# Optimization experiments

Measured on AMD Instinct MI355X. Metric: run time of the kernel, lower is better.

The kernel has to match this reference:

```python
import jax, jax.numpy as jnp
import numpy as np

IN_CH, HID, OUT = 128, 128, 47

def _sage_conv(x_src, x_dst, src, dst, n_dst, Wl, bl, Wr):
    # mean aggregation of source features onto destination nodes
    msg_sum = jax.ops.segment_sum(x_src[src], dst, num_segments=n_dst)
    deg = jax.ops.segment_sum(jnp.ones((src.shape[0],), x_src.dtype), dst, num_segments=n_dst)
    agg = msg_sum / jnp.maximum(deg, 1.0)[:, None]
    return agg @ Wl + bl + x_dst @ Wr


def setup_inputs() -> dict:
    key = jax.random.key(0)
    ks = jax.random.split(key, 12)
    N0, N1, N2 = 200000, 100000, 20000
    E0, E1 = 1600000, 320000
    def glorot(k, fan_in, fan_out):
        s = jnp.sqrt(6.0 / (fan_in + fan_out))
        return jax.random.uniform(k, (fan_in, fan_out), jnp.float32, -s, s)
    return {
        'x': jax.random.normal(ks[0], (N0, IN_CH), jnp.float32),
        'src0': jax.random.randint(ks[1], (E0,), 0, N0),
        'dst0': jax.random.randint(ks[2], (E0,), 0, N1),
        'src1': jax.random.randint(ks[3], (E1,), 0, N1),
        'dst1': jax.random.randint(ks[4], (E1,), 0, N2),
        'n1': N1,
        'n2': N2,
        'Wl0': glorot(ks[5], IN_CH, HID),
        'bl0': jnp.zeros((HID,), jnp.float32),
        'Wr0': glorot(ks[6], IN_CH, HID),
        'Wl1': glorot(ks[7], HID, OUT),
        'bl1': jnp.zeros((OUT,), jnp.float32),
        'Wr1': glorot(ks[8], HID, OUT),
    }


def reference(x, src0, dst0, src1, dst1, n1, n2, Wl0, bl0, Wr0, Wl1, bl1, Wr1):
    # layer 0: bipartite SAGEConv + relu (dropout is identity in eval mode)
    h = _sage_conv(x, x[:n1], src0, dst0, n1, Wl0, bl0, Wr0)
    h = jax.nn.relu(h)
    # layer 1: SAGEConv to output classes
    out = _sage_conv(h, h[:n2], src1, dst1, n2, Wl1, bl1, Wr1)
    return jax.nn.log_softmax(out, axis=-1)
```

## Files before the change

### kernel.cpp

```cpp
#include <hip/hip_runtime.h>
#include <hip/hip_bf16.h>
#include <math.h>

#define N1_ROWS 100000
#define N2_ROWS 20000
#define CH 128
#define OUTC 47
#define BSH 7
#define BROWS 128
#define CAP 2560
#define NBMX 1024
#define SCHUNK 4096

typedef __attribute__((ext_vector_type(8))) short short8;
typedef __attribute__((ext_vector_type(4))) float floatx4;

__device__ inline ushort f2b(float f) {
    union { __hip_bfloat16 b; ushort u; } cv;
    cv.b = __float2bfloat16(f);
    return cv.u;
}
__device__ inline float b2f_lo(uint u) { return __uint_as_float(u << 16); }
__device__ inline float b2f_hi(uint u) { return __uint_as_float(u & 0xffff0000u); }

__device__ inline void scatter_body(
    const int* __restrict__ src, const int* __restrict__ dst,
    uint* __restrict__ gcur, uint* __restrict__ ebuf, int E, int NB,
    int sb, uint* hist, uint* runb)
{
    const int base = sb * SCHUNK;
    const int t = threadIdx.x;

    uint d[16], s[16];
    bool ok[4];
    #pragma unroll
    for (int j = 0; j < 4; ++j) {
        int e = base + j * 1024 + t * 4;
        ok[j] = (e < E);
        if (ok[j]) {
            uint4 dv = *(const uint4*)(dst + e);
            uint4 sv = *(const uint4*)(src + e);
            d[j*4+0] = dv.x; d[j*4+1] = dv.y; d[j*4+2] = dv.z; d[j*4+3] = dv.w;
            s[j*4+0] = sv.x; s[j*4+1] = sv.y; s[j*4+2] = sv.z; s[j*4+3] = sv.w;
        }
    }

    for (int b = t; b < NBMX; b += 256) hist[b] = 0;
    __syncthreads();
    #pragma unroll
    for (int j = 0; j < 4; ++j)
        if (ok[j]) {
            #pragma unroll
            for (int k = 0; k < 4; ++k) atomicAdd(&hist[d[j*4+k] >> BSH], 1u);
        }
    __syncthreads();
    for (int b = t; b < NB; b += 256) {
        uint c = hist[b];
        runb[b] = c ? atomicAdd(&gcur[b], c) : 0u;
        hist[b] = 0;
    }
    __syncthreads();
    #pragma unroll
    for (int j = 0; j < 4; ++j)
        if (ok[j]) {
            #pragma unroll
            for (int k = 0; k < 4; ++k) {
                uint dd = d[j*4+k];
                uint b = dd >> BSH;
                uint off = runb[b] + atomicAdd(&hist[b], 1u);
                if (off < CAP)
                    ebuf[(size_t)b * CAP + off] = ((dd & (BROWS - 1u)) << 18) | s[j*4+k];
            }
        }
}

__global__ __launch_bounds__(256) void prep(
    const float* __restrict__ x, ushort* __restrict__ xb, int n4,
    const int* __restrict__ src0, const int* __restrict__ dst0,
    uint* __restrict__ gcur0, uint* __restrict__ ebuf0, int E0, int NB0,
    const int* __restrict__ src1, const int* __restrict__ dst1,
    uint* __restrict__ gcur1, uint* __restrict__ ebuf1, int E1, int NB1,
    const float* __restrict__ Wl0, const float* __restrict__ Wr0,
    const float* __restrict__ Wl1, const float* __restrict__ Wr1,
    const float* __restrict__ bl1,
    ushort* __restrict__ W0p, ushort* __restrict__ W1p, float* __restrict__ bl1p,
    int CB, int S0, int S1)
{
    __shared__ uint hist[NBMX];
    __shared__ uint runb[NBMX];
    int blk = blockIdx.x;
    if (blk < S0) {
        scatter_body(src0, dst0, gcur0, ebuf0, E0, NB0, blk, hist, runb);
    } else if (blk < S0 + S1) {
        scatter_body(src1, dst1, gcur1, ebuf1, E1, NB1, blk - S0, hist, runb);
    } else if (blk == S0 + S1) {
        int t = threadIdx.x;
        for (int c = t; c < 4096; c += 256) {
            int n = c & 127; int kb = (c >> 7) & 15; int p = c >> 11;
            const float* W = p ? Wr0 : Wl0;
            __align__(16) ushort tmp[8];
            #pragma unroll
            for (int i = 0; i < 8; ++i) tmp[i] = f2b(W[(kb * 8 + i) * CH + n]);
            *(uint4*)(W0p + (size_t)c * 8) = *(const uint4*)tmp;
        }
    } else if (blk == S0 + S1 + 1) {
        int t = threadIdx.x;
        for (int c = t; c < 1536; c += 256) {
            int n = c % 48; int kb = (c / 48) & 15; int p = c / 768;
            const float* W = p ? Wr1 : Wl1;
            __align__(16) ushort tmp[8];
            #pragma unroll
            for (int i = 0; i < 8; ++i)
                tmp[i] = (n < OUTC) ? f2b(W[(kb * 8 + i) * OUTC + n]) : (ushort)0;
            *(uint4*)(W1p + (size_t)c * 8) = *(const uint4*)tmp;
        }
        if (t < 48) bl1p[t] = (t < OUTC) ? bl1[t] : -3.0e38f;
    } else {
        int i = (blk - S0 - S1 - 2) * 256 + threadIdx.x;
        if (i < n4) {
            float4 v = ((const float4*)x)[i];
            ushort4 o;
            o.x = f2b(v.x); o.y = f2b(v.y); o.z = f2b(v.z); o.w = f2b(v.w);
            ((ushort4*)xb)[i] = o;
        }
    }
}

__global__ __launch_bounds__(512) void csr_gather(
    const uint* __restrict__ ebuf0, const uint* __restrict__ gcur0,
    const ushort* __restrict__ xb, ushort* __restrict__ aggb, int NB0, int n1,
    const uint* __restrict__ ebuf1, const uint* __restrict__ gcur1,
    int* __restrict__ idx1, int* __restrict__ deg1, int* __restrict__ rs1,
    int NB1, int n2)
{
    int t = threadIdx.x;
    __shared__ uint idxl[CAP];
    __shared__ uint hist[BROWS];
    __shared__ uint sc[BROWS];
    __shared__ uint lrs[BROWS];
    __shared__ uint degl[BROWS];
    __shared__ uint psc[256];

    int b = blockIdx.x;
    if (b < NB0) {
        uint cnt = gcur0[b]; if (cnt > CAP) cnt = CAP;
        size_t bin = (size_t)b * CAP;

        if (t < BROWS) hist[t] = 0;
        __syncthreads();
        for (uint i0 = 0; i0 < cnt; i0 += 2048) {
            uint i = i0 + t * 4;
            uint v0 = 0, v1 = 0, v2 = 0, v3 = 0; int nv = 0;
            if (i + 3 < cnt) {
                uint4 vv = *(const uint4*)(ebuf0 + bin + i);
                v0 = vv.x; v1 = vv.y; v2 = vv.z; v3 = vv.w; nv = 4;
            } else if (i < cnt) {
                nv = (int)(cnt - i);
                v0 = ebuf0[bin + i];
                if (nv > 1) v1 = ebuf0[bin + i + 1];
                if (nv > 2) v2 = ebuf0[bin + i + 2];
            }
            if (nv > 0) atomicAdd(&hist[v0 >> 18], 1u);
            if (nv > 1) atomicAdd(&hist[v1 >> 18], 1u);
            if (nv > 2) atomicAdd(&hist[v2 >> 18], 1u);
            if (nv > 3) atomicAdd(&hist[v3 >> 18], 1u);
        }
        __syncthreads();
        uint hv = 0;
        if (t < BROWS) { hv = hist[t]; sc[t] = hv; }
        __syncthreads();
        for (int off = 1; off < BROWS; off <<= 1) {
            uint val = 0;
            if (t < BROWS && t >= off) val = sc[t - off];
            __syncthreads();
            if (t < BROWS) sc[t] += val;
            __syncthreads();
        }
        if (t < BROWS) { lrs[t] = sc[t] - hv; degl[t] = hv; hist[t] = 0; }
        __syncthreads();
        for (uint i0 = 0; i0 < cnt; i0 += 2048) {
            uint i = i0 + t * 4;
            uint v0 = 0, v1 = 0, v2 = 0, v3 = 0; int nv = 0;
            if (i + 3 < cnt) {
                uint4 vv = *(const uint4*)(ebuf0 + bin + i);
                v0 = vv.x; v1 = vv.y; v2 = vv.z; v3 = vv.w; nv = 4;
            } else if (i < cnt) {
                nv = (int)(cnt - i);
                v0 = ebuf0[bin + i];
                if (nv > 1) v1 = ebuf0[bin + i + 1];
                if (nv > 2) v2 = ebuf0[bin + i + 2];
            }
            if (nv > 0) { uint r = v0 >> 18; idxl[lrs[r] + atomicAdd(&hist[r], 1u)] = v0 & 0x3FFFFu; }
            if (nv > 1) { uint r = v1 >> 18; idxl[lrs[r] + atomicAdd(&hist[r], 1u)] = v1 & 0x3FFFFu; }
            if (nv > 2) { uint r = v2 >> 18; idxl[lrs[r] + atomicAdd(&hist[r], 1u)] = v2 & 0x3FFFFu; }
            if (nv > 3) { uint r = v3 >> 18; idxl[lrs[r] + atomicAdd(&hist[r], 1u)] = v3 & 0x3FFFFu; }
        }
        __syncthreads();

        int wave = t >> 6, lane = t & 63;
        const int g  = lane >> 4;
        const int sl = lane & 15;
        const int gid = wave * 4 + g;
        const uint4* x4 = (const uint4*)xb;
        #pragma unroll 1
        for (int k = 0; k < 4; ++k) {
            int r = gid + 32 * k;
            int row = (b << BSH) + r;
            if (row >= n1) break;
            int start = (int)lrs[r];
            int cnt_r = (int)degl[r];
            float a0 = 0.f, a1 = 0.f, a2 = 0.f, a3 = 0.f;
            float a4 = 0.f, a5 = 0.f, a6 = 0.f, a7 = 0.f;
            int i = 0;
            for (; i + 3 < cnt_r; i += 4) {
                uint s0 = idxl[start + i];
                uint s1 = idxl[start + i + 1];
                uint s2 = idxl[start + i + 2];
                uint s3 = idxl[start + i + 3];
                uint4 v0 = x4[(size_t)s0 * 16 + sl];
                uint4 v1 = x4[(size_t)s1 * 16 + sl];
                uint4 v2 = x4[(size_t)s2 * 16 + sl];
                uint4 v3 = x4[(size_t)s3 * 16 + sl];
                a0 += (b2f_lo(v0.x) + b2f_lo(v1.x)) + (b2f_lo(v2.x) + b2f_lo(v3.x));
                a1 += (b2f_hi(v0.x) + b2f_hi(v1.x)) + (b2f_hi(v2.x) + b2f_hi(v3.x));
                a2 += (b2f_lo(v0.y) + b2f_lo(v1.y)) + (b2f_lo(v2.y) + b2f_lo(v3.y));
                a3 += (b2f_hi(v0.y) + b2f_hi(v1.y)) + (b2f_hi(v2.y) + b2f_hi(v3.y));
                a4 += (b2f_lo(v0.z) + b2f_lo(v1.z)) + (b2f_lo(v2.z) + b2f_lo(v3.z));
                a5 += (b2f_hi(v0.z) + b2f_hi(v1.z)) + (b2f_hi(v2.z) + b2f_hi(v3.z));
                a6 += (b2f_lo(v0.w) + b2f_lo(v1.w)) + (b2f_lo(v2.w) + b2f_lo(v3.w));
                a7 += (b2f_hi(v0.w) + b2f_hi(v1.w)) + (b2f_hi(v2.w) + b2f_hi(v3.w));
            }
            for (; i < cnt_r; ++i) {
                uint s0 = idxl[start + i];
                uint4 v0 = x4[(size_t)s0 * 16 + sl];
                a0 += b2f_lo(v0.x); a1 += b2f_hi(v0.x);
                a2 += b2f_lo(v0.y); a3 += b2f_hi(v0.y);
                a4 += b2f_lo(v0.z); a5 += b2f_hi(v0.z);
                a6 += b2f_lo(v0.w); a7 += b2f_hi(v0.w);
            }
            float inv = 1.0f / fmaxf((float)cnt_r, 1.0f);
            uint4 o;
            o.x = (uint)f2b(a0 * inv) | ((uint)f2b(a1 * inv) << 16);
            o.y = (uint)f2b(a2 * inv) | ((uint)f2b(a3 * inv) << 16);
            o.z = (uint)f2b(a4 * inv) | ((uint)f2b(a5 * inv) << 16);
            o.w = (uint)f2b(a6 * inv) | ((uint)f2b(a7 * inv) << 16);
            ((uint4*)aggb)[(size_t)row * 16 + sl] = o;
        }
    } else {
        b -= NB0;
        if (t < 256) {
            uint c = (t < NB1) ? gcur1[t] : 0u; if (c > CAP) c = CAP;
            psc[t] = c;
        }
        __syncthreads();
        for (int off = 1; off < 256; off <<= 1) {
            uint val = 0;
            if (t < 256 && t >= off) val = psc[t - off];
            __syncthreads();
            if (t < 256) psc[t] += val;
            __syncthreads();
        }
        uint cnt = gcur1[b]; if (cnt > CAP) cnt = CAP;
        uint bout = psc[b] - cnt;
        size_t bin = (size_t)b * CAP;
        int row0 = b << BSH;
        int nrows = n2 - row0; if (nrows > BROWS) nrows = BROWS;

        if (t < BROWS) hist[t] = 0;
        __syncthreads();
        for (uint i0 = 0; i0 < cnt; i0 += 2048) {
            uint i = i0 + t * 4;
            uint v0 = 0, v1 = 0, v2 = 0, v3 = 0; int nv = 0;
            if (i + 3 < cnt) {
                uint4 vv = *(const uint4*)(ebuf1 + bin + i);
                v0 = vv.x; v1 = vv.y; v2 = vv.z; v3 = vv.w; nv = 4;
            } else if (i < cnt) {
                nv = (int)(cnt - i);
                v0 = ebuf1[bin + i];
                if (nv > 1) v1 = ebuf1[bin + i + 1];
                if (nv > 2) v2 = ebuf1[bin + i + 2];
            }
            if (nv > 0) atomicAdd(&hist[v0 >> 18], 1u);
            if (nv > 1) atomicAdd(&hist[v1 >> 18], 1u);
            if (nv > 2) atomicAdd(&hist[v2 >> 18], 1u);
            if (nv > 3) atomicAdd(&hist[v3 >> 18], 1u);
        }
        __syncthreads();
        uint hv = 0;
        if (t < BROWS) { hv = hist[t]; sc[t] = hv; }
        __syncthreads();
        for (int off = 1; off < BROWS; off <<= 1) {
            uint val = 0;
            if (t < BROWS && t >= off) val = sc[t - off];
            __syncthreads();
            if (t < BROWS) sc[t] += val;
            __syncthreads();
        }
        if (t < BROWS) {
            uint lb = sc[t] - hv;
            lrs[t] = lb;
            if (t < nrows) { deg1[row0 + t] = (int)hv; rs1[row0 + t] = (int)(bout + lb); }
            hist[t] = 0;
        }
        __syncthreads();
        for (uint i0 = 0; i0 < cnt; i0 += 2048) {
            uint i = i0 + t * 4;
            uint v0 = 0, v1 = 0, v2 = 0, v3 = 0; int nv = 0;
            if (i + 3 < cnt) {
                uint4 vv = *(const uint4*)(ebuf1 + bin + i);
                v0 = vv.x; v1 = vv.y; v2 = vv.z; v3 = vv.w; nv = 4;
            } else if (i < cnt) {
                nv = (int)(cnt - i);
                v0 = ebuf1[bin + i];
                if (nv > 1) v1 = ebuf1[bin + i + 1];
                if (nv > 2) v2 = ebuf1[bin + i + 2];
            }
            if (nv > 0) { uint r = v0 >> 18; idxl[lrs[r] + atomicAdd(&hist[r], 1u)] = v0 & 0x3FFFFu; }
            if (nv > 1) { uint r = v1 >> 18; idxl[lrs[r] + atomicAdd(&hist[r], 1u)] = v1 & 0x3FFFFu; }
            if (nv > 2) { uint r = v2 >> 18; idxl[lrs[r] + atomicAdd(&hist[r], 1u)] = v2 & 0x3FFFFu; }
            if (nv > 3) { uint r = v3 >> 18; idxl[lrs[r] + atomicAdd(&hist[r], 1u)] = v3 & 0x3FFFFu; }
        }
        __syncthreads();
        for (uint i = t; i < cnt; i += 512) idx1[bout + i] = (int)idxl[i];
    }
}

__global__ __launch_bounds__(256) void gather_mean_bb(
    const ushort* __restrict__ xb,
    const int* __restrict__ idx,
    const int* __restrict__ rs,
    const int* __restrict__ deg,
    ushort* __restrict__ aggb,
    int n)
{
    int lane = threadIdx.x & 63;
    int wave = threadIdx.x >> 6;
    const int g  = lane >> 4;
    const int sl = lane & 15;
    int row = blockIdx.x * 16 + wave * 4 + g;
    if (row >= n) return;
    int start = rs[row];
    int cnt = deg[row];
    const uint4* x4 = (const uint4*)xb;
    float a0 = 0.f, a1 = 0.f, a2 = 0.f, a3 = 0.f;
    float a4 = 0.f, a5 = 0.f, a6 = 0.f, a7 = 0.f;
    int i = 0;
    for (; i + 3 < cnt; i += 4) {
        int s0 = idx[start + i];
        int s1 = idx[start + i + 1];
        int s2 = idx[start + i + 2];
        int s3 = idx[start + i + 3];
        uint4 v0 = x4[(size_t)s0 * 16 + sl];
        uint4 v1 = x4[(size_t)s1 * 16 + sl];
        uint4 v2 = x4[(size_t)s2 * 16 + sl];
        uint4 v3 = x4[(size_t)s3 * 16 + sl];
        a0 += (b2f_lo(v0.x) + b2f_lo(v1.x)) + (b2f_lo(v2.x) + b2f_lo(v3.x));
        a1 += (b2f_hi(v0.x) + b2f_hi(v1.x)) + (b2f_hi(v2.x) + b2f_hi(v3.x));
        a2 += (b2f_lo(v0.y) + b2f_lo(v1.y)) + (b2f_lo(v2.y) + b2f_lo(v3.y));
        a3 += (b2f_hi(v0.y) + b2f_hi(v1.y)) + (b2f_hi(v2.y) + b2f_hi(v3.y));
        a4 += (b2f_lo(v0.z) + b2f_lo(v1.z)) + (b2f_lo(v2.z) + b2f_lo(v3.z));
        a5 += (b2f_hi(v0.z) + b2f_hi(v1.z)) + (b2f_hi(v2.z) + b2f_hi(v3.z));
        a6 += (b2f_lo(v0.w) + b2f_lo(v1.w)) + (b2f_lo(v2.w) + b2f_lo(v3.w));
        a7 += (b2f_hi(v0.w) + b2f_hi(v1.w)) + (b2f_hi(v2.w) + b2f_hi(v3.w));
    }
    for (; i < cnt; ++i) {
        int s0 = idx[start + i];
        uint4 v0 = x4[(size_t)s0 * 16 + sl];
        a0 += b2f_lo(v0.x); a1 += b2f_hi(v0.x);
        a2 += b2f_lo(v0.y); a3 += b2f_hi(v0.y);
        a4 += b2f_lo(v0.z); a5 += b2f_hi(v0.z);
        a6 += b2f_lo(v0.w); a7 += b2f_hi(v0.w);
    }
    float inv = 1.0f / fmaxf((float)cnt, 1.0f);
    uint4 o;
    o.x = (uint)f2b(a0 * inv) | ((uint)f2b(a1 * inv) << 16);
    o.y = (uint)f2b(a2 * inv) | ((uint)f2b(a3 * inv) << 16);
    o.z = (uint)f2b(a4 * inv) | ((uint)f2b(a5 * inv) << 16);
    o.w = (uint)f2b(a6 * inv) | ((uint)f2b(a7 * inv) << 16);
    ((uint4*)aggb)[(size_t)row * 16 + sl] = o;
}

#define TM 128
__global__ __launch_bounds__(256) void gemm_mfma(
    const ushort* __restrict__ Apan,
    const ushort* __restrict__ Bpan,
    const ushort* __restrict__ Wp,
    const float* __restrict__ bias,
    ushort* __restrict__ H,
    int rows)
{
    __shared__ __align__(16) ushort As[16384];
    __shared__ __align__(16) ushort Ws[16384];

    const int tid = threadIdx.x;
    const int lane = tid & 63;
    const int wave = tid >> 6;
    const int q = lane >> 4;
    const int ln = lane & 15;
    const int rbase = blockIdx.x * TM;
    const int mrow = wave * 32;

    floatx4 acc[2][8];
    #pragma unroll
    for (int i = 0; i < 2; ++i)
        #pragma unroll
        for (int j = 0; j < 8; ++j)
            acc[i][j] = (floatx4)0.0f;

    #pragma unroll 1
    for (int phase = 0; phase < 2; ++phase) {
        const ushort* Ag = phase ? Bpan : Apan;

        {
            int m0 = tid & 15;
            int c  = tid >> 4;
            #pragma unroll
            for (int j = 0; j < 8; ++j) {
                int m = m0 + 16 * j;
                uint4 v = *(const uint4*)(Ag + (size_t)(rbase + m) * CH + c * 8);
                *(uint4*)(As + ((size_t)c * 128 + m) * 8) = v;
            }
        }
        {
            const uint4* Wg4 = (const uint4*)(Wp + phase * 16384);
            uint4* Ws4 = (uint4*)Ws;
            for (int i = tid; i < 2048; i += 256) Ws4[i] = Wg4[i];
        }
        __syncthreads();

        #pragma unroll
        for (int k = 0; k < 4; ++k) {
            int kb = k * 4 + q;
            short8 b[8];
            #pragma unroll
            for (int nt = 0; nt < 8; ++nt)
                b[nt] = *(const short8*)(Ws + ((size_t)kb * 128 + nt * 16 + ln) * 8);
            #pragma unroll
            for (int mt = 0; mt < 2; ++mt) {
                short8 a = *(const short8*)(As + ((size_t)kb * 128 + mrow + mt * 16 + ln) * 8);
                #pragma unroll
                for (int nt = 0; nt < 8; ++nt)
                    acc[mt][nt] = __builtin_amdgcn_mfma_f32_16x16x32_bf16(
                        a, b[nt], acc[mt][nt], 0, 0, 0);
            }
        }
        __syncthreads();
    }

    float bj[8];
    #pragma unroll
    for (int nt = 0; nt < 8; ++nt) bj[nt] = bias[nt * 16 + ln];

    #pragma unroll
    for (int mt = 0; mt < 2; ++mt) {
        #pragma unroll
        for (int r = 0; r < 4; ++r) {
            int grow = rbase + mrow + mt * 16 + q * 4 + r;
            if (grow < rows) {
                #pragma unroll
                for (int nt = 0; nt < 8; ++nt) {
                    float v = acc[mt][nt][r] + bj[nt];
                    v = fmaxf(v, 0.0f);
                    H[(size_t)grow * CH + nt * 16 + ln] = f2b(v);
                }
            }
        }
    }
}

__global__ __launch_bounds__(256) void gemm_mfma_l1(
    const ushort* __restrict__ Apan,
    const ushort* __restrict__ Bpan,
    const ushort* __restrict__ Wp,
    const float* __restrict__ biasp,
    float* __restrict__ out,
    int rows)
{
    __shared__ __align__(16) ushort As[16384];
    __shared__ __align__(16) ushort Ws[6144];

    const int tid = threadIdx.x;
    const int lane = tid & 63;
    const int wave = tid >> 6;
    const int q = lane >> 4;
    const int ln = lane & 15;
    const int rbase = blockIdx.x * TM;
    const int mrow = wave * 32;

    floatx4 acc[2][3];
    #pragma unroll
    for (int i = 0; i < 2; ++i)
        #pragma unroll
        for (int j = 0; j < 3; ++j)
            acc[i][j] = (floatx4)0.0f;

    #pragma unroll 1
    for (int phase = 0; phase < 2; ++phase) {
        const ushort* Ag = phase ? Bpan : Apan;
        {
            int m0 = tid & 15;
            int c  = tid >> 4;
            #pragma unroll
            for (int j = 0; j < 8; ++j) {
                int m = m0 + 16 * j;
                uint4 v = *(const uint4*)(Ag + (size_t)(rbase + m) * CH + c * 8);
                *(uint4*)(As + ((size_t)c * 128 + m) * 8) = v;
            }
        }
        {
            const uint4* Wg4 = (const uint4*)(Wp + phase * 6144);
            uint4* Ws4 = (uint4*)Ws;
            for (int i = tid; i < 768; i += 256) Ws4[i] = Wg4[i];
        }
        __syncthreads();

        #pragma unroll
        for (int k = 0; k < 4; ++k) {
            int kb = k * 4 + q;
            short8 b0 = *(const short8*)(Ws + ((size_t)kb * 48 +  0 + ln) * 8);
            short8 b1 = *(const short8*)(Ws + ((size_t)kb * 48 + 16 + ln) * 8);
            short8 b2 = *(const short8*)(Ws + ((size_t)kb * 48 + 32 + ln) * 8);
            #pragma unroll
            for (int mt = 0; mt < 2; ++mt) {
                short8 a = *(const short8*)(As + ((size_t)kb * 128 + mrow + mt * 16 + ln) * 8);
                acc[mt][0] = __builtin_amdgcn_mfma_f32_16x16x32_bf16(a, b0, acc[mt][0], 0, 0, 0);
                acc[mt][1] = __builtin_amdgcn_mfma_f32_16x16x32_bf16(a, b1, acc[mt][1], 0, 0, 0);
                acc[mt][2] = __builtin_amdgcn_mfma_f32_16x16x32_bf16(a, b2, acc[mt][2], 0, 0, 0);
            }
        }
        __syncthreads();
    }

    float b0 = biasp[ln], b1 = biasp[16 + ln], b2 = biasp[32 + ln];

    #pragma unroll
    for (int mt = 0; mt < 2; ++mt) {
        #pragma unroll
        for (int r = 0; r < 4; ++r) {
            int grow = rbase + mrow + mt * 16 + q * 4 + r;
            float v0 = acc[mt][0][r] + b0;
            float v1 = acc[mt][1][r] + b1;
            float v2 = acc[mt][2][r] + b2;
            float mx = fmaxf(v0, fmaxf(v1, v2));
            #pragma unroll
            for (int off = 1; off < 16; off <<= 1) mx = fmaxf(mx, __shfl_xor(mx, off));
            float s = expf(v0 - mx) + expf(v1 - mx) + expf(v2 - mx);
            #pragma unroll
            for (int off = 1; off < 16; off <<= 1) s += __shfl_xor(s, off);
            float ls = mx + logf(s);
            if (grow < rows) {
                out[(size_t)grow * OUTC + ln] = v0 - ls;
                out[(size_t)grow * OUTC + 16 + ln] = v1 - ls;
                if (32 + ln < OUTC) out[(size_t)grow * OUTC + 32 + ln] = v2 - ls;
            }
        }
    }
}

extern "C" void kernel_launch(void* const* d_in, const int* in_sizes, int n_in,
                              void* d_out, int out_size, void* d_ws, size_t ws_size,
                              hipStream_t stream) {
    const float* x    = (const float*)d_in[0];
    const int*   src0 = (const int*)d_in[1];
    const int*   dst0 = (const int*)d_in[2];
    const int*   src1 = (const int*)d_in[3];
    const int*   dst1 = (const int*)d_in[4];
    const float* Wl0  = (const float*)d_in[7];
    const float* bl0  = (const float*)d_in[8];
    const float* Wr0  = (const float*)d_in[9];
    const float* Wl1  = (const float*)d_in[10];
    const float* bl1  = (const float*)d_in[11];
    const float* Wr1  = (const float*)d_in[12];
    float* out = (float*)d_out;

    const int E0 = in_sizes[1];
    const int E1 = in_sizes[3];
    const int n0 = in_sizes[0] / CH;
    const int n1 = N1_ROWS, n2 = N2_ROWS;
    const int n1pad = ((n1 + TM - 1) / TM) * TM;
    const int n2pad = ((n2 + TM - 1) / TM) * TM;
    const int NB0 = (n1 + BROWS - 1) >> BSH;
    const int NB1 = (n2 + BROWS - 1) >> BSH;

    ushort* xb   = (ushort*)d_ws;
    ushort* aggb = xb + (size_t)n0 * CH;
    ushort* h    = aggb + (size_t)n1pad * CH;
    ushort* W0p  = h + (size_t)n1 * CH;
    ushort* W1p  = W0p + 32768;
    float*  bl1p = (float*)(W1p + 12288);
    int*    idx1 = (int*)(bl1p + 48);
    int*    deg1 = idx1 + E1;
    int*    rs1  = deg1 + n2;
    uint*   gcur0 = (uint*)(rs1 + n2);
    uint*   gcur1 = gcur0 + NBMX;

    uint* ebuf0 = (uint*)h;
    uint* ebuf1 = (uint*)h + (size_t)NB0 * CAP;
    ushort* agg1b = aggb;

    const int n4 = n0 * CH / 4;
    const int CB = (n4 + 255) / 256;
    const int S0 = (E0 + SCHUNK - 1) / SCHUNK;
    const int S1 = (E1 + SCHUNK - 1) / SCHUNK;

    hipMemsetAsync(gcur0, 0, 2 * NBMX * sizeof(uint), stream);
    prep<<<S0 + S1 + 2 + CB, 256, 0, stream>>>(
        x, xb, n4,
        src0, dst0, gcur0, ebuf0, E0, NB0,
        src1, dst1, gcur1, ebuf1, E1, NB1,
        Wl0, Wr0, Wl1, Wr1, bl1, W0p, W1p, bl1p,
        CB, S0, S1);
    csr_gather<<<NB0 + NB1, 512, 0, stream>>>(
        ebuf0, gcur0, xb, aggb, NB0, n1,
        ebuf1, gcur1, idx1, deg1, rs1, NB1, n2);
    gemm_mfma<<<n1pad / TM, 256, 0, stream>>>(aggb, xb, W0p, bl0, h, n1);
    gather_mean_bb<<<(n2 + 15) / 16, 256, 0, stream>>>(h, idx1, rs1, deg1, agg1b, n2);
    gemm_mfma_l1<<<n2pad / TM, 256, 0, stream>>>(agg1b, h, W1p, bl1p, out, n2);
}
```

Before: 316.2 us.

## Fuse per-block CSR gather with MFMA GEMM for both SAGE layers

Each 128-row destination block now builds its local CSR, gathers and averages neighbor features straight into shared memory in the MFMA A-layout, then runs the two-phase GEMM (aggregate @ Wl plus self @ Wr) in the same kernel. This removes the global round trip of the aggregated features and the layer-1 idx/deg/rowstart buffers, and cuts four kernel launches to two. The edge buffers move to their own workspace region because h is now written while they are still needed. In exchange each block uses much more shared memory (about 64KB extra), which lowers occupancy during the latency-bound gather, and the GEMM now uses 8 waves with 16 rows each.

```diff
diff --git a/kernel.cpp b/kernel.cpp
--- a/kernel.cpp
+++ b/kernel.cpp
@@ -126,12 +126,12 @@
     }
 }
 
-__global__ __launch_bounds__(512) void csr_gather(
-    const uint* __restrict__ ebuf0, const uint* __restrict__ gcur0,
-    const ushort* __restrict__ xb, ushort* __restrict__ aggb, int NB0, int n1,
-    const uint* __restrict__ ebuf1, const uint* __restrict__ gcur1,
-    int* __restrict__ idx1, int* __restrict__ deg1, int* __restrict__ rs1,
-    int NB1, int n2)
+__global__ __launch_bounds__(512) void fused0(
+    const uint* __restrict__ ebuf, const uint* __restrict__ gcur,
+    const ushort* __restrict__ xb,
+    const ushort* __restrict__ Wp,
+    const float* __restrict__ bias,
+    ushort* __restrict__ H, int n1)
 {
     int t = threadIdx.x;
     __shared__ uint idxl[CAP];
@@ -139,74 +139,80 @@
     __shared__ uint sc[BROWS];
     __shared__ uint lrs[BROWS];
     __shared__ uint degl[BROWS];
-    __shared__ uint psc[256];
+    __shared__ __align__(16) ushort As[16384];
+    __shared__ __align__(16) ushort Ws[16384];
 
     int b = blockIdx.x;
-    if (b < NB0) {
-        uint cnt = gcur0[b]; if (cnt > CAP) cnt = CAP;
-        size_t bin = (size_t)b * CAP;
-
-        if (t < BROWS) hist[t] = 0;
+    uint cnt = gcur[b]; if (cnt > CAP) cnt = CAP;
+    size_t bin = (size_t)b * CAP;
+
+    {
+        const uint4* Wg4 = (const uint4*)Wp;
+        uint4* Ws4 = (uint4*)Ws;
+        for (int i = t; i < 2048; i += 512) Ws4[i] = Wg4[i];
+    }
+
+    if (t < BROWS) hist[t] = 0;
+    __syncthreads();
+    for (uint i0 = 0; i0 < cnt; i0 += 2048) {
+        uint i = i0 + t * 4;
+        uint v0 = 0, v1 = 0, v2 = 0, v3 = 0; int nv = 0;
+        if (i + 3 < cnt) {
+            uint4 vv = *(const uint4*)(ebuf + bin + i);
+            v0 = vv.x; v1 = vv.y; v2 = vv.z; v3 = vv.w; nv = 4;
+        } else if (i < cnt) {
+            nv = (int)(cnt - i);
+            v0 = ebuf[bin + i];
+            if (nv > 1) v1 = ebuf[bin + i + 1];
+            if (nv > 2) v2 = ebuf[bin + i + 2];
+        }
+        if (nv > 0) atomicAdd(&hist[v0 >> 18], 1u);
+        if (nv > 1) atomicAdd(&hist[v1 >> 18], 1u);
+        if (nv > 2) atomicAdd(&hist[v2 >> 18], 1u);
+        if (nv > 3) atomicAdd(&hist[v3 >> 18], 1u);
+    }
+    __syncthreads();
+    uint hv = 0;
+    if (t < BROWS) { hv = hist[t]; sc[t] = hv; }
+    __syncthreads();
+    for (int off = 1; off < BROWS; off <<= 1) {
+        uint val = 0;
+        if (t < BROWS && t >= off) val = sc[t - off];
         __syncthreads();
-        for (uint i0 = 0; i0 < cnt; i0 += 2048) {
-            uint i = i0 + t * 4;
-            uint v0 = 0, v1 = 0, v2 = 0, v3 = 0; int nv = 0;
-            if (i + 3 < cnt) {
-                uint4 vv = *(const uint4*)(ebuf0 + bin + i);
-                v0 = vv.x; v1 = vv.y; v2 = vv.z; v3 = vv.w; nv = 4;
-            } else if (i < cnt) {
-                nv = (int)(cnt - i);
-                v0 = ebuf0[bin + i];
-                if (nv > 1) v1 = ebuf0[bin + i + 1];
-                if (nv > 2) v2 = ebuf0[bin + i + 2];
-            }
-            if (nv > 0) atomicAdd(&hist[v0 >> 18], 1u);
-            if (nv > 1) atomicAdd(&hist[v1 >> 18], 1u);
-            if (nv > 2) atomicAdd(&hist[v2 >> 18], 1u);
-            if (nv > 3) atomicAdd(&hist[v3 >> 18], 1u);
-        }
+        if (t < BROWS) sc[t] += val;
         __syncthreads();
-        uint hv = 0;
-        if (t < BROWS) { hv = hist[t]; sc[t] = hv; }
-        __syncthreads();
-        for (int off = 1; off < BROWS; off <<= 1) {
-            uint val = 0;
-            if (t < BROWS && t >= off) val = sc[t - off];
-            __syncthreads();
-            if (t < BROWS) sc[t] += val;
-            __syncthreads();
-        }
-        if (t < BROWS) { lrs[t] = sc[t] - hv; degl[t] = hv; hist[t] = 0; }
-        __syncthreads();
-        for (uint i0 = 0; i0 < cnt; i0 += 2048) {
-            uint i = i0 + t * 4;
-            uint v0 = 0, v1 = 0, v2 = 0, v3 = 0; int nv = 0;
-            if (i + 3 < cnt) {
-                uint4 vv = *(const uint4*)(ebuf0 + bin + i);
-                v0 = vv.x; v1 = vv.y; v2 = vv.z; v3 = vv.w; nv = 4;
-            } else if (i < cnt) {
-                nv = (int)(cnt - i);
-                v0 = ebuf0[bin + i];
-                if (nv > 1) v1 = ebuf0[bin + i + 1];
-                if (nv > 2) v2 = ebuf0[bin + i + 2];
-            }
-            if (nv > 0) { uint r = v0 >> 18; idxl[lrs[r] + atomicAdd(&hist[r], 1u)] = v0 & 0x3FFFFu; }
-            if (nv > 1) { uint r = v1 >> 18; idxl[lrs[r] + atomicAdd(&hist[r], 1u)] = v1 & 0x3FFFFu; }
-            if (nv > 2) { uint r = v2 >> 18; idxl[lrs[r] + atomicAdd(&hist[r], 1u)] = v2 & 0x3FFFFu; }
-            if (nv > 3) { uint r = v3 >> 18; idxl[lrs[r] + atomicAdd(&hist[r], 1u)] = v3 & 0x3FFFFu; }
-        }
-        __syncthreads();
-
-        int wave = t >> 6, lane = t & 63;
-        const int g  = lane >> 4;
-        const int sl = lane & 15;
-        const int gid = wave * 4 + g;
-        const uint4* x4 = (const uint4*)xb;
-        #pragma unroll 1
-        for (int k = 0; k < 4; ++k) {
-            int r = gid + 32 * k;
-            int row = (b << BSH) + r;
-            if (row >= n1) break;
+    }
+    if (t < BROWS) { lrs[t] = sc[t] - hv; degl[t] = hv; hist[t] = 0; }
+    __syncthreads();
+    for (uint i0 = 0; i0 < cnt; i0 += 2048) {
+        uint i = i0 + t * 4;
+        uint v0 = 0, v1 = 0, v2 = 0, v3 = 0; int nv = 0;
+        if (i + 3 < cnt) {
+            uint4 vv = *(const uint4*)(ebuf + bin + i);
+            v0 = vv.x; v1 = vv.y; v2 = vv.z; v3 = vv.w; nv = 4;
+        } else if (i < cnt) {
+            nv = (int)(cnt - i);
+            v0 = ebuf[bin + i];
+            if (nv > 1) v1 = ebuf[bin + i + 1];
+            if (nv > 2) v2 = ebuf[bin + i + 2];
+        }
+        if (nv > 0) { uint r = v0 >> 18; idxl[lrs[r] + atomicAdd(&hist[r], 1u)] = v0 & 0x3FFFFu; }
+        if (nv > 1) { uint r = v1 >> 18; idxl[lrs[r] + atomicAdd(&hist[r], 1u)] = v1 & 0x3FFFFu; }
+        if (nv > 2) { uint r = v2 >> 18; idxl[lrs[r] + atomicAdd(&hist[r], 1u)] = v2 & 0x3FFFFu; }
+        if (nv > 3) { uint r = v3 >> 18; idxl[lrs[r] + atomicAdd(&hist[r], 1u)] = v3 & 0x3FFFFu; }
+    }
+    __syncthreads();
+
+    int wave = t >> 6, lane = t & 63;
+    const int g  = lane >> 4;
+    const int sl = lane & 15;
+    const int gid = wave * 4 + g;
+    const uint4* x4 = (const uint4*)xb;
+    #pragma unroll 1
+    for (int k = 0; k < 4; ++k) {
+        int r = gid + 32 * k;
+        int row = (b << BSH) + r;
+        if (row < n1) {
             int start = (int)lrs[r];
             int cnt_r = (int)degl[r];
             float a0 = 0.f, a1 = 0.f, a2 = 0.f, a3 = 0.f;
@@ -244,315 +250,254 @@
             o.y = (uint)f2b(a2 * inv) | ((uint)f2b(a3 * inv) << 16);
             o.z = (uint)f2b(a4 * inv) | ((uint)f2b(a5 * inv) << 16);
             o.w = (uint)f2b(a6 * inv) | ((uint)f2b(a7 * inv) << 16);
-            ((uint4*)aggb)[(size_t)row * 16 + sl] = o;
-        }
-    } else {
-        b -= NB0;
-        if (t < 256) {
-            uint c = (t < NB1) ? gcur1[t] : 0u; if (c > CAP) c = CAP;
-            psc[t] = c;
-        }
-        __syncthreads();
-        for (int off = 1; off < 256; off <<= 1) {
-            uint val = 0;
-            if (t < 256 && t >= off) val = psc[t - off];
-            __syncthreads();
-            if (t < 256) psc[t] += val;
-            __syncthreads();
-        }
-        uint cnt = gcur1[b]; if (cnt > CAP) cnt = CAP;
-        uint bout = psc[b] - cnt;
-        size_t bin = (size_t)b * CAP;
-        int row0 = b << BSH;
-        int nrows = n2 - row0; if (nrows > BROWS) nrows = BROWS;
-
-        if (t < BROWS) hist[t] = 0;
-        __syncthreads();
-        for (uint i0 = 0; i0 < cnt; i0 += 2048) {
-            uint i = i0 + t * 4;
-            uint v0 = 0, v1 = 0, v2 = 0, v3 = 0; int nv = 0;
-            if (i + 3 < cnt) {
-                uint4 vv = *(const uint4*)(ebuf1 + bin + i);
-                v0 = vv.x; v1 = vv.y; v2 = vv.z; v3 = vv.w; nv = 4;
-            } else if (i < cnt) {
-                nv = (int)(cnt - i);
-                v0 = ebuf1[bin + i];
-                if (nv > 1) v1 = ebuf1[bin + i + 1];
-                if (nv > 2) v2 = ebuf1[bin + i + 2];
-            }
-            if (nv > 0) atomicAdd(&hist[v0 >> 18], 1u);
-            if (nv > 1) atomicAdd(&hist[v1 >> 18], 1u);
-            if (nv > 2) atomicAdd(&hist[v2 >> 18], 1u);
-            if (nv > 3) atomicAdd(&hist[v3 >> 18], 1u);
-        }
-        __syncthreads();
-        uint hv = 0;
-        if (t < BROWS) { hv = hist[t]; sc[t] = hv; }
-        __syncthreads();
-        for (int off = 1; off < BROWS; off <<= 1) {
-            uint val = 0;
-            if (t < BROWS && t >= off) val = sc[t - off];
-            __syncthreads();
-            if (t < BROWS) sc[t] += val;
-            __syncthreads();
-        }
-        if (t < BROWS) {
-            uint lb = sc[t] - hv;
-            lrs[t] = lb;
-            if (t < nrows) { deg1[row0 + t] = (int)hv; rs1[row0 + t] = (int)(bout + lb); }
-            hist[t] = 0;
-        }
-        __syncthreads();
-        for (uint i0 = 0; i0 < cnt; i0 += 2048) {
-            uint i = i0 + t * 4;
-            uint v0 = 0, v1 = 0, v2 = 0, v3 = 0; int nv = 0;
-            if (i + 3 < cnt) {
-                uint4 vv = *(const uint4*)(ebuf1 + bin + i);
-                v0 = vv.x; v1 = vv.y; v2 = vv.z; v3 = vv.w; nv = 4;
-            } else if (i < cnt) {
-                nv = (int)(cnt - i);
-                v0 = ebuf1[bin + i];
-                if (nv > 1) v1 = ebuf1[bin + i + 1];
-                if (nv > 2) v2 = ebuf1[bin + i + 2];
-            }
-            if (nv > 0) { uint r = v0 >> 18; idxl[lrs[r] + atomicAdd(&hist[r], 1u)] = v0 & 0x3FFFFu; }
-            if (nv > 1) { uint r = v1 >> 18; idxl[lrs[r] + atomicAdd(&hist[r], 1u)] = v1 & 0x3FFFFu; }
-            if (nv > 2) { uint r = v2 >> 18; idxl[lrs[r] + atomicAdd(&hist[r], 1u)] = v2 & 0x3FFFFu; }
-            if (nv > 3) { uint r = v3 >> 18; idxl[lrs[r] + atomicAdd(&hist[r], 1u)] = v3 & 0x3FFFFu; }
-        }
-        __syncthreads();
-        for (uint i = t; i < cnt; i += 512) idx1[bout + i] = (int)idxl[i];
-    }
-}
-
-__global__ __launch_bounds__(256) void gather_mean_bb(
-    const ushort* __restrict__ xb,
-    const int* __restrict__ idx,
-    const int* __restrict__ rs,
-    const int* __restrict__ deg,
-    ushort* __restrict__ aggb,
-    int n)
-{
-    int lane = threadIdx.x & 63;
-    int wave = threadIdx.x >> 6;
-    const int g  = lane >> 4;
-    const int sl = lane & 15;
-    int row = blockIdx.x * 16 + wave * 4 + g;
-    if (row >= n) return;
-    int start = rs[row];
-    int cnt = deg[row];
-    const uint4* x4 = (const uint4*)xb;
-    float a0 = 0.f, a1 = 0.f, a2 = 0.f, a3 = 0.f;
-    float a4 = 0.f, a5 = 0.f, a6 = 0.f, a7 = 0.f;
-    int i = 0;
-    for (; i + 3 < cnt; i += 4) {
-        int s0 = idx[start + i];
-        int s1 = idx[start + i + 1];
-        int s2 = idx[start + i + 2];
-        int s3 = idx[start + i + 3];
-        uint4 v0 = x4[(size_t)s0 * 16 + sl];
-        uint4 v1 = x4[(size_t)s1 * 16 + sl];
-        uint4 v2 = x4[(size_t)s2 * 16 + sl];
-        uint4 v3 = x4[(size_t)s3 * 16 + sl];
-        a0 += (b2f_lo(v0.x) + b2f_lo(v1.x)) + (b2f_lo(v2.x) + b2f_lo(v3.x));
-        a1 += (b2f_hi(v0.x) + b2f_hi(v1.x)) + (b2f_hi(v2.x) + b2f_hi(v3.x));
-        a2 += (b2f_lo(v0.y) + b2f_lo(v1.y)) + (b2f_lo(v2.y) + b2f_lo(v3.y));
-        a3 += (b2f_hi(v0.y) + b2f_hi(v1.y)) + (b2f_hi(v2.y) + b2f_hi(v3.y));
-        a4 += (b2f_lo(v0.z) + b2f_lo(v1.z)) + (b2f_lo(v2.z) + b2f_lo(v3.z));
-        a5 += (b2f_hi(v0.z) + b2f_hi(v1.z)) + (b2f_hi(v2.z) + b2f_hi(v3.z));
-        a6 += (b2f_lo(v0.w) + b2f_lo(v1.w)) + (b2f_lo(v2.w) + b2f_lo(v3.w));
-        a7 += (b2f_hi(v0.w) + b2f_hi(v1.w)) + (b2f_hi(v2.w) + b2f_hi(v3.w));
-    }
-    for (; i < cnt; ++i) {
-        int s0 = idx[start + i];
-        uint4 v0 = x4[(size_t)s0 * 16 + sl];
-        a0 += b2f_lo(v0.x); a1 += b2f_hi(v0.x);
-        a2 += b2f_lo(v0.y); a3 += b2f_hi(v0.y);
-        a4 += b2f_lo(v0.z); a5 += b2f_hi(v0.z);
-        a6 += b2f_lo(v0.w); a7 += b2f_hi(v0.w);
-    }
-    float inv = 1.0f / fmaxf((float)cnt, 1.0f);
-    uint4 o;
-    o.x = (uint)f2b(a0 * inv) | ((uint)f2b(a1 * inv) << 16);
-    o.y = (uint)f2b(a2 * inv) | ((uint)f2b(a3 * inv) << 16);
-    o.z = (uint)f2b(a4 * inv) | ((uint)f2b(a5 * inv) << 16);
-    o.w = (uint)f2b(a6 * inv) | ((uint)f2b(a7 * inv) << 16);
-    ((uint4*)aggb)[(size_t)row * 16 + sl] = o;
-}
-
-#define TM 128
-__global__ __launch_bounds__(256) void gemm_mfma(
-    const ushort* __restrict__ Apan,
-    const ushort* __restrict__ Bpan,
-    const ushort* __restrict__ Wp,
-    const float* __restrict__ bias,
-    ushort* __restrict__ H,
-    int rows)
-{
-    __shared__ __align__(16) ushort As[16384];
-    __shared__ __align__(16) ushort Ws[16384];
-
-    const int tid = threadIdx.x;
-    const int lane = tid & 63;
-    const int wave = tid >> 6;
-    const int q = lane >> 4;
-    const int ln = lane & 15;
-    const int rbase = blockIdx.x * TM;
-    const int mrow = wave * 32;
-
-    floatx4 acc[2][8];
-    #pragma unroll
-    for (int i = 0; i < 2; ++i)
-        #pragma unroll
-        for (int j = 0; j < 8; ++j)
-            acc[i][j] = (floatx4)0.0f;
+            *(uint4*)(As + ((size_t)sl * 128 + r) * 8) = o;
+        }
+    }
+
+    const int q = g, ln = sl;
+    const int rbase = b << BSH;
+    const int mrow = wave * 16;
+    floatx4 acc[8];
+    #pragma unroll
+    for (int nt = 0; nt < 8; ++nt) acc[nt] = (floatx4)0.0f;
 
     #pragma unroll 1
     for (int phase = 0; phase < 2; ++phase) {
-        const ushort* Ag = phase ? Bpan : Apan;
-
-        {
-            int m0 = tid & 15;
-            int c  = tid >> 4;
-            #pragma unroll
-            for (int j = 0; j < 8; ++j) {
-                int m = m0 + 16 * j;
-                uint4 v = *(const uint4*)(Ag + (size_t)(rbase + m) * CH + c * 8);
-                *(uint4*)(As + ((size_t)c * 128 + m) * 8) = v;
-            }
-        }
-        {
-            const uint4* Wg4 = (const uint4*)(Wp + phase * 16384);
-            uint4* Ws4 = (uint4*)Ws;
-            for (int i = tid; i < 2048; i += 256) Ws4[i] = Wg4[i];
+        if (phase == 1) {
+            __syncthreads();
+            {
+                int m0 = t & 15, c = (t >> 4) & 15, jb = (t >> 8) * 4;
+                #pragma unroll
+                for (int j = 0; j < 4; ++j) {
+                    int m = m0 + 16 * (jb + j);
+                    uint4 v = *(const uint4*)(xb + (size_t)(rbase + m) * CH + c * 8);
+                    *(uint4*)(As + ((size_t)c * 128 + m) * 8) = v;
+                }
+            }
+            {
+                const uint4* Wg4 = (const uint4*)(Wp + 16384);
+                uint4* Ws4 = (uint4*)Ws;
+                for (int i = t; i < 2048; i += 512) Ws4[i] = Wg4[i];
+            }
         }
         __syncthreads();
-
         #pragma unroll
         for (int k = 0; k < 4; ++k) {
             int kb = k * 4 + q;
-            short8 b[8];
+            short8 bb[8];
             #pragma unroll
             for (int nt = 0; nt < 8; ++nt)
-                b[nt] = *(const short8*)(Ws + ((size_t)kb * 128 + nt * 16 + ln) * 8);
-            #pragma unroll
-            for (int mt = 0; mt < 2; ++mt) {
-                short8 a = *(const short8*)(As + ((size_t)kb * 128 + mrow + mt * 16 + ln) * 8);
-                #pragma unroll
-                for (int nt = 0; nt < 8; ++nt)
-                    acc[mt][nt] = __builtin_amdgcn_mfma_f32_16x16x32_bf16(
-                        a, b[nt], acc[mt][nt], 0, 0, 0);
-            }
-        }
-        __syncthreads();
+                bb[nt] = *(const short8*)(Ws + ((size_t)kb * 128 + nt * 16 + ln) * 8);
+            short8 a = *(const short8*)(As + ((size_t)kb * 128 + mrow + ln) * 8);
+            #pragma unroll
+            for (int nt = 0; nt < 8; ++nt)
+                acc[nt] = __builtin_amdgcn_mfma_f32_16x16x32_bf16(a, bb[nt], acc[nt], 0, 0, 0);
+        }
     }
 
     float bj[8];
     #pragma unroll
     for (int nt = 0; nt < 8; ++nt) bj[nt] = bias[nt * 16 + ln];
-
-    #pragma unroll
-    for (int mt = 0; mt < 2; ++mt) {
-        #pragma unroll
-        for (int r = 0; r < 4; ++r) {
-            int grow = rbase + mrow + mt * 16 + q * 4 + r;
-            if (grow < rows) {
-                #pragma unroll
-                for (int nt = 0; nt < 8; ++nt) {
-                    float v = acc[mt][nt][r] + bj[nt];
-                    v = fmaxf(v, 0.0f);
-                    H[(size_t)grow * CH + nt * 16 + ln] = f2b(v);
-                }
+    #pragma unroll
+    for (int r = 0; r < 4; ++r) {
+        int grow = rbase + mrow + q * 4 + r;
+        if (grow < n1) {
+            #pragma unroll
+            for (int nt = 0; nt < 8; ++nt) {
+                float v = acc[nt][r] + bj[nt];
+                v = fmaxf(v, 0.0f);
+                H[(size_t)grow * CH + nt * 16 + ln] = f2b(v);
             }
         }
     }
 }
 
-__global__ __launch_bounds__(256) void gemm_mfma_l1(
-    const ushort* __restrict__ Apan,
-    const ushort* __restrict__ Bpan,
+__global__ __launch_bounds__(512) void fused1(
+    const uint* __restrict__ ebuf, const uint* __restrict__ gcur,
+    const ushort* __restrict__ hb,
     const ushort* __restrict__ Wp,
     const float* __restrict__ biasp,
-    float* __restrict__ out,
-    int rows)
+    float* __restrict__ out, int n2)
 {
+    int t = threadIdx.x;
+    __shared__ uint idxl[CAP];
+    __shared__ uint hist[BROWS];
+    __shared__ uint sc[BROWS];
+    __shared__ uint lrs[BROWS];
+    __shared__ uint degl[BROWS];
     __shared__ __align__(16) ushort As[16384];
     __shared__ __align__(16) ushort Ws[6144];
 
-    const int tid = threadIdx.x;
-    const int lane = tid & 63;
-    const int wave = tid >> 6;
-    const int q = lane >> 4;
-    const int ln = lane & 15;
-    const int rbase = blockIdx.x * TM;
-    const int mrow = wave * 32;
-
-    floatx4 acc[2][3];
-    #pragma unroll
-    for (int i = 0; i < 2; ++i)
-        #pragma unroll
-        for (int j = 0; j < 3; ++j)
-            acc[i][j] = (floatx4)0.0f;
+    int b = blockIdx.x;
+    uint cnt = gcur[b]; if (cnt > CAP) cnt = CAP;
+    size_t bin = (size_t)b * CAP;
+
+    {
+        const uint4* Wg4 = (const uint4*)Wp;
+        uint4* Ws4 = (uint4*)Ws;
+        for (int i = t; i < 768; i += 512) Ws4[i] = Wg4[i];
+    }
+
+    if (t < BROWS) hist[t] = 0;
+    __syncthreads();
+    for (uint i0 = 0; i0 < cnt; i0 += 2048) {
+        uint i = i0 + t * 4;
+        uint v0 = 0, v1 = 0, v2 = 0, v3 = 0; int nv = 0;
+        if (i + 3 < cnt) {
+            uint4 vv = *(const uint4*)(ebuf + bin + i);
+            v0 = vv.x; v1 = vv.y; v2 = vv.z; v3 = vv.w; nv = 4;
+        } else if (i < cnt) {
+            nv = (int)(cnt - i);
+            v0 = ebuf[bin + i];
+            if (nv > 1) v1 = ebuf[bin + i + 1];
+            if (nv > 2) v2 = ebuf[bin + i + 2];
+        }
+        if (nv > 0) atomicAdd(&hist[v0 >> 18], 1u);
+        if (nv > 1) atomicAdd(&hist[v1 >> 18], 1u);
+        if (nv > 2) atomicAdd(&hist[v2 >> 18], 1u);
+        if (nv > 3) atomicAdd(&hist[v3 >> 18], 1u);
+    }
+    __syncthreads();
+    uint hv = 0;
+    if (t < BROWS) { hv = hist[t]; sc[t] = hv; }
+    __syncthreads();
+    for (int off = 1; off < BROWS; off <<= 1) {
+        uint val = 0;
+        if (t < BROWS && t >= off) val = sc[t - off];
+        __syncthreads();
+        if (t < BROWS) sc[t] += val;
+        __syncthreads();
+    }
+    if (t < BROWS) { lrs[t] = sc[t] - hv; degl[t] = hv; hist[t] = 0; }
+    __syncthreads();
+    for (uint i0 = 0; i0 < cnt; i0 += 2048) {
+        uint i = i0 + t * 4;
+        uint v0 = 0, v1 = 0, v2 = 0, v3 = 0; int nv = 0;
+        if (i + 3 < cnt) {
+            uint4 vv = *(const uint4*)(ebuf + bin + i);
+            v0 = vv.x; v1 = vv.y; v2 = vv.z; v3 = vv.w; nv = 4;
+        } else if (i < cnt) {
+            nv = (int)(cnt - i);
+            v0 = ebuf[bin + i];
+            if (nv > 1) v1 = ebuf[bin + i + 1];
+            if (nv > 2) v2 = ebuf[bin + i + 2];
+        }
+        if (nv > 0) { uint r = v0 >> 18; idxl[lrs[r] + atomicAdd(&hist[r], 1u)] = v0 & 0x3FFFFu; }
+        if (nv > 1) { uint r = v1 >> 18; idxl[lrs[r] + atomicAdd(&hist[r], 1u)] = v1 & 0x3FFFFu; }
+        if (nv > 2) { uint r = v2 >> 18; idxl[lrs[r] + atomicAdd(&hist[r], 1u)] = v2 & 0x3FFFFu; }
+        if (nv > 3) { uint r = v3 >> 18; idxl[lrs[r] + atomicAdd(&hist[r], 1u)] = v3 & 0x3FFFFu; }
+    }
+    __syncthreads();
+
+    int wave = t >> 6, lane = t & 63;
+    const int g  = lane >> 4;
+    const int sl = lane & 15;
+    const int gid = wave * 4 + g;
+    const uint4* x4 = (const uint4*)hb;
+    #pragma unroll 1
+    for (int k = 0; k < 4; ++k) {
+        int r = gid + 32 * k;
+        int row = (b << BSH) + r;
+        if (row < n2) {
+            int start = (int)lrs[r];
+            int cnt_r = (int)degl[r];
+            float a0 = 0.f, a1 = 0.f, a2 = 0.f, a3 = 0.f;
+            float a4 = 0.f, a5 = 0.f, a6 = 0.f, a7 = 0.f;
+            int i = 0;
+            for (; i + 3 < cnt_r; i += 4) {
+                uint s0 = idxl[start + i];
+                uint s1 = idxl[start + i + 1];
+                uint s2 = idxl[start + i + 2];
+                uint s3 = idxl[start + i + 3];
+                uint4 v0 = x4[(size_t)s0 * 16 + sl];
+                uint4 v1 = x4[(size_t)s1 * 16 + sl];
+                uint4 v2 = x4[(size_t)s2 * 16 + sl];
+                uint4 v3 = x4[(size_t)s3 * 16 + sl];
+                a0 += (b2f_lo(v0.x) + b2f_lo(v1.x)) + (b2f_lo(v2.x) + b2f_lo(v3.x));
+                a1 += (b2f_hi(v0.x) + b2f_hi(v1.x)) + (b2f_hi(v2.x) + b2f_hi(v3.x));
+                a2 += (b2f_lo(v0.y) + b2f_lo(v1.y)) + (b2f_lo(v2.y) + b2f_lo(v3.y));
+                a3 += (b2f_hi(v0.y) + b2f_hi(v1.y)) + (b2f_hi(v2.y) + b2f_hi(v3.y));
+                a4 += (b2f_lo(v0.z) + b2f_lo(v1.z)) + (b2f_lo(v2.z) + b2f_lo(v3.z));
+                a5 += (b2f_hi(v0.z) + b2f_hi(v1.z)) + (b2f_hi(v2.z) + b2f_hi(v3.z));
+                a6 += (b2f_lo(v0.w) + b2f_lo(v1.w)) + (b2f_lo(v2.w) + b2f_lo(v3.w));
+                a7 += (b2f_hi(v0.w) + b2f_hi(v1.w)) + (b2f_hi(v2.w) + b2f_hi(v3.w));
+            }
+            for (; i < cnt_r; ++i) {
+                uint s0 = idxl[start + i];
+                uint4 v0 = x4[(size_t)s0 * 16 + sl];
+                a0 += b2f_lo(v0.x); a1 += b2f_hi(v0.x);
+                a2 += b2f_lo(v0.y); a3 += b2f_hi(v0.y);
+                a4 += b2f_lo(v0.z); a5 += b2f_hi(v0.z);
+                a6 += b2f_lo(v0.w); a7 += b2f_hi(v0.w);
+            }
+            float inv = 1.0f / fmaxf((float)cnt_r, 1.0f);
+            uint4 o;
+            o.x = (uint)f2b(a0 * inv) | ((uint)f2b(a1 * inv) << 16);
+            o.y = (uint)f2b(a2 * inv) | ((uint)f2b(a3 * inv) << 16);
+            o.z = (uint)f2b(a4 * inv) | ((uint)f2b(a5 * inv) << 16);
+            o.w = (uint)f2b(a6 * inv) | ((uint)f2b(a7 * inv) << 16);
+            *(uint4*)(As + ((size_t)sl * 128 + r) * 8) = o;
+        }
+    }
+
+    const int q = g, ln = sl;
+    const int rbase = b << BSH;
+    const int mrow = wave * 16;
+    floatx4 acc[3];
+    #pragma unroll
+    for (int nt = 0; nt < 3; ++nt) acc[nt] = (floatx4)0.0f;
 
     #pragma unroll 1
     for (int phase = 0; phase < 2; ++phase) {
-        const ushort* Ag = phase ? Bpan : Apan;
-        {
-            int m0 = tid & 15;
-            int c  = tid >> 4;
-            #pragma unroll
-            for (int j = 0; j < 8; ++j) {
-                int m = m0 + 16 * j;
-                uint4 v = *(const uint4*)(Ag + (size_t)(rbase + m) * CH + c * 8);
-                *(uint4*)(As + ((size_t)c * 128 + m) * 8) = v;
-            }
-        }
-        {
-            const uint4* Wg4 = (const uint4*)(Wp + phase * 6144);
-            uint4* Ws4 = (uint4*)Ws;
-            for (int i = tid; i < 768; i += 256) Ws4[i] = Wg4[i];
+        if (phase == 1) {
+            __syncthreads();
+            {
+                int m0 = t & 15, c = (t >> 4) & 15, jb = (t >> 8) * 4;
+                #pragma unroll
+                for (int j = 0; j < 4; ++j) {
+                    int m = m0 + 16 * (jb + j);
+                    uint4 v = *(const uint4*)(hb + (size_t)(rbase + m) * CH + c * 8);
+                    *(uint4*)(As + ((size_t)c * 128 + m) * 8) = v;
+                }
+            }
+            {
+                const uint4* Wg4 = (const uint4*)(Wp + 6144);
+                uint4* Ws4 = (uint4*)Ws;
+                for (int i = t; i < 768; i += 512) Ws4[i] = Wg4[i];
+            }
         }
         __syncthreads();
-
         #pragma unroll
         for (int k = 0; k < 4; ++k) {
             int kb = k * 4 + q;
             short8 b0 = *(const short8*)(Ws + ((size_t)kb * 48 +  0 + ln) * 8);
             short8 b1 = *(const short8*)(Ws + ((size_t)kb * 48 + 16 + ln) * 8);
             short8 b2 = *(const short8*)(Ws + ((size_t)kb * 48 + 32 + ln) * 8);
-            #pragma unroll
-            for (int mt = 0; mt < 2; ++mt) {
-                short8 a = *(const short8*)(As + ((size_t)kb * 128 + mrow + mt * 16 + ln) * 8);
-                acc[mt][0] = __builtin_amdgcn_mfma_f32_16x16x32_bf16(a, b0, acc[mt][0], 0, 0, 0);
-                acc[mt][1] = __builtin_amdgcn_mfma_f32_16x16x32_bf16(a, b1, acc[mt][1], 0, 0, 0);
-                acc[mt][2] = __builtin_amdgcn_mfma_f32_16x16x32_bf16(a, b2, acc[mt][2], 0, 0, 0);
-            }
-        }
-        __syncthreads();
+            short8 a = *(const short8*)(As + ((size_t)kb * 128 + mrow + ln) * 8);
+            acc[0] = __builtin_amdgcn_mfma_f32_16x16x32_bf16(a, b0, acc[0], 0, 0, 0);
+            acc[1] = __builtin_amdgcn_mfma_f32_16x16x32_bf16(a, b1, acc[1], 0, 0, 0);
+            acc[2] = __builtin_amdgcn_mfma_f32_16x16x32_bf16(a, b2, acc[2], 0, 0, 0);
+        }
     }
 
     float b0 = biasp[ln], b1 = biasp[16 + ln], b2 = biasp[32 + ln];
-
-    #pragma unroll
-    for (int mt = 0; mt < 2; ++mt) {
+    #pragma unroll
+    for (int r = 0; r < 4; ++r) {
+        int grow = rbase + mrow + q * 4 + r;
+        float v0 = acc[0][r] + b0;
+        float v1 = acc[1][r] + b1;
+        float v2 = acc[2][r] + b2;
+        float mx = fmaxf(v0, fmaxf(v1, v2));
         #pragma unroll
-        for (int r = 0; r < 4; ++r) {
-            int grow = rbase + mrow + mt * 16 + q * 4 + r;
-            float v0 = acc[mt][0][r] + b0;
-            float v1 = acc[mt][1][r] + b1;
-            float v2 = acc[mt][2][r] + b2;
-            float mx = fmaxf(v0, fmaxf(v1, v2));
-            #pragma unroll
-            for (int off = 1; off < 16; off <<= 1) mx = fmaxf(mx, __shfl_xor(mx, off));
-            float s = expf(v0 - mx) + expf(v1 - mx) + expf(v2 - mx);
-            #pragma unroll
-            for (int off = 1; off < 16; off <<= 1) s += __shfl_xor(s, off);
-            float ls = mx + logf(s);
-            if (grow < rows) {
-                out[(size_t)grow * OUTC + ln] = v0 - ls;
-                out[(size_t)grow * OUTC + 16 + ln] = v1 - ls;
-                if (32 + ln < OUTC) out[(size_t)grow * OUTC + 32 + ln] = v2 - ls;
-            }
+        for (int off = 1; off < 16; off <<= 1) mx = fmaxf(mx, __shfl_xor(mx, off));
+        float s = expf(v0 - mx) + expf(v1 - mx) + expf(v2 - mx);
+        #pragma unroll
+        for (int off = 1; off < 16; off <<= 1) s += __shfl_xor(s, off);
+        float ls = mx + logf(s);
+        if (grow < n2) {
+            out[(size_t)grow * OUTC + ln] = v0 - ls;
+            out[(size_t)grow * OUTC + 16 + ln] = v1 - ls;
+            if (32 + ln < OUTC) out[(size_t)grow * OUTC + 32 + ln] = v2 - ls;
         }
     }
 }
@@ -577,26 +522,18 @@
     const int E1 = in_sizes[3];
     const int n0 = in_sizes[0] / CH;
     const int n1 = N1_ROWS, n2 = N2_ROWS;
-    const int n1pad = ((n1 + TM - 1) / TM) * TM;
-    const int n2pad = ((n2 + TM - 1) / TM) * TM;
     const int NB0 = (n1 + BROWS - 1) >> BSH;
     const int NB1 = (n2 + BROWS - 1) >> BSH;
 
     ushort* xb   = (ushort*)d_ws;
-    ushort* aggb = xb + (size_t)n0 * CH;
-    ushort* h    = aggb + (size_t)n1pad * CH;
+    ushort* h    = xb + (size_t)n0 * CH;
     ushort* W0p  = h + (size_t)n1 * CH;
     ushort* W1p  = W0p + 32768;
     float*  bl1p = (float*)(W1p + 12288);
-    int*    idx1 = (int*)(bl1p + 48);
-    int*    deg1 = idx1 + E1;
-    int*    rs1  = deg1 + n2;
-    uint*   gcur0 = (uint*)(rs1 + n2);
+    uint*   gcur0 = (uint*)(bl1p + 48);
     uint*   gcur1 = gcur0 + NBMX;
-
-    uint* ebuf0 = (uint*)h;
-    uint* ebuf1 = (uint*)h + (size_t)NB0 * CAP;
-    ushort* agg1b = aggb;
+    uint*   ebuf0 = gcur1 + NBMX;
+    uint*   ebuf1 = ebuf0 + (size_t)NB0 * CAP;
 
     const int n4 = n0 * CH / 4;
     const int CB = (n4 + 255) / 256;
@@ -610,10 +547,6 @@
         src1, dst1, gcur1, ebuf1, E1, NB1,
         Wl0, Wr0, Wl1, Wr1, bl1, W0p, W1p, bl1p,
         CB, S0, S1);
-    csr_gather<<<NB0 + NB1, 512, 0, stream>>>(
-        ebuf0, gcur0, xb, aggb, NB0, n1,
-        ebuf1, gcur1, idx1, deg1, rs1, NB1, n2);
-    gemm_mfma<<<n1pad / TM, 256, 0, stream>>>(aggb, xb, W0p, bl0, h, n1);
-    gather_mean_bb<<<(n2 + 15) / 16, 256, 0, stream>>>(h, idx1, rs1, deg1, agg1b, n2);
-    gemm_mfma_l1<<<n2pad / TM, 256, 0, stream>>>(agg1b, h, W1p, bl1p, out, n2);
+    fused0<<<NB0, 512, 0, stream>>>(ebuf0, gcur0, xb, W0p, bl0, h, n1);
+    fused1<<<NB1, 512, 0, stream>>>(ebuf1, gcur1, h, W1p, bl1p, out, n2);
 }
```

New measurement: 299.5 us, median of 2. -5.3%, faster.
